# Optimization experiments

Measured on AMD Instinct MI355X. Metric: run time of the kernel, lower is better.

## Reference

```python
import jax, jax.numpy as jnp
import numpy as np

NUM_SITES_X = 2048
NUM_SITES_Y = 4096
NUM_CLB_SITES = 6_000_000
NUM_SLICE_SITES = 6_000_000
NUM_SITES = NUM_SITES_X * NUM_SITES_Y  # global flattened site-id space


def setup_inputs() -> dict:
    key = jax.random.key(0)
    k1, k2, k3, k4 = jax.random.split(key, 4)
    # CLB slice site ids (x*num_sites_y + y), sorted as produced from the column-major fabric scan
    slice_sites = jnp.sort(
        jax.random.randint(k1, (NUM_SLICE_SITES,), 0, NUM_SITES, dtype=jnp.int32))
    # per-CLB-site signature count; >0 means the site already has instances committed
    site_det_sig_idx = jax.random.randint(
        k2, (NUM_CLB_SITES,), 0, 4, dtype=jnp.int32)
    # compact CLB address -> global site id map (monotone by construction in the original)
    addr2site_map = jnp.sort(
        jax.random.randint(k3, (NUM_CLB_SITES,), 0, NUM_SITES, dtype=jnp.int32))
    # per-slice-site legalization score (site_det_score analogue)
    site_scores = jax.random.normal(k4, (NUM_SLICE_SITES,), dtype=jnp.float32)
    return {
        "slice_sites": slice_sites,
        "site_det_sig_idx": site_det_sig_idx,
        "addr2site_map": addr2site_map,
        "site_scores": site_scores,
    }


def _remaining_mask(slice_sites, site_det_sig_idx, addr2site_map):
    """Faithful jit-friendly version of compute_remaining_slice_sites.

    torch/np original:
      assigned = addr2site_map[site_det_sig_idx > 0]
      mask[np.in1d(slice_sites, assigned)] = True; return ~mask
    We avoid the data-dependent boolean gather by replacing unassigned
    entries with a -1 sentinel (site ids are >= 0), sorting, and doing a
    vectorized membership test via searchsorted.
    """
    n = addr2site_map.shape[0]
    assigned = jnp.where(site_det_sig_idx > 0, addr2site_map, jnp.int32(-1))
    assigned_sorted = jnp.sort(assigned)  # sentinels land at the front
    pos = jnp.searchsorted(assigned_sorted, slice_sites, side="left")
    pos = jnp.clip(pos, 0, n - 1)
    found = assigned_sorted[pos] == slice_sites  # in1d membership
    return ~found  # True where the slice site is still available


def reference(slice_sites, site_det_sig_idx, addr2site_map, site_scores):
    remaining = _remaining_mask(slice_sites, site_det_sig_idx, addr2site_map)
    # scores of still-available candidate sites (zeros where already assigned)
    avail_scores = jnp.where(remaining, site_scores, jnp.zeros((), site_scores.dtype))
    return remaining, avail_scores
```

## Files before the change

### kernel.cpp

```cpp
#include <hip/hip_runtime.h>


typedef int   v4i __attribute__((ext_vector_type(4)));
typedef float v4f __attribute__((ext_vector_type(4)));

static constexpr int WORDS_PER_BLOCK = 128;
static constexpr int SITES_PER_BLOCK = 4096;
static constexpr int BIN_SHIFT       = 12;
static constexpr int GRID            = 2048;
static constexpr int BLOCK           = 256;

__device__ __forceinline__ void transitions(
    const int* __restrict__ x, int* __restrict__ bnd, int n, int t)
{
    const int s = t * 4;
    if (s >= n) return;
    int v[4];
    int cnt;
    if (s + 4 <= n) {
        v4i a = __builtin_nontemporal_load((const v4i*)(x + s));
        v[0] = a.x; v[1] = a.y; v[2] = a.z; v[3] = a.w;
        cnt = 4;
    } else {
        cnt = n - s;
        for (int j = 0; j < cnt; ++j) v[j] = x[s + j];
    }
    int pbin = (s == 0) ? -1 : (x[s - 1] >> BIN_SHIFT);
    for (int j = 0; j < cnt; ++j) {
        const int i = s + j;
        const int cbin = v[j] >> BIN_SHIFT;
        for (int b = pbin + 1; b <= cbin; ++b) bnd[b] = i;
        if (i == n - 1)
            for (int b = cbin + 1; b <= GRID; ++b) bnd[b] = n;
        pbin = cbin;
    }
}

__global__ __launch_bounds__(BLOCK) void bounds_kernel(
    const int* __restrict__ ss, const int* __restrict__ a2s,
    int* __restrict__ pb, int* __restrict__ eb, int n_slice, int n_clb)
{
    const int t = blockIdx.x * BLOCK + threadIdx.x;
    transitions(ss,  pb, n_slice, t);
    transitions(a2s, eb, n_clb,  t);
}

__global__ __launch_bounds__(BLOCK) void fused_kernel(
    const int*   __restrict__ ss,
    const int*   __restrict__ sig,
    const int*   __restrict__ a2s,
    const float* __restrict__ sc,
    const int*   __restrict__ eb,
    const int*   __restrict__ pb,
    float*       __restrict__ rem,
    float*       __restrict__ avail,
    int n_clb)
{
    __shared__ unsigned int lbm[WORDS_PER_BLOCK];

    const int g        = blockIdx.x;
    const int siteBase = g * SITES_PER_BLOCK;
    const int siteEnd  = siteBase + SITES_PER_BLOCK;

    for (int w = threadIdx.x; w < WORDS_PER_BLOCK; w += BLOCK) lbm[w] = 0u;

    const int e0 = eb[g], e1 = eb[g + 1];
    const int p0 = pb[g], p1 = pb[g + 1];

    __syncthreads();

    const int mstart = e0 & ~3;
    for (int s = mstart + threadIdx.x * 8; s < e1; s += BLOCK * 8) {
        int av[8], gv[8];
        if (s + 8 <= n_clb) {
            v4i a0 = __builtin_nontemporal_load((const v4i*)(a2s + s));
            v4i a1 = __builtin_nontemporal_load((const v4i*)(a2s + s + 4));
            v4i g0 = __builtin_nontemporal_load((const v4i*)(sig + s));
            v4i g1 = __builtin_nontemporal_load((const v4i*)(sig + s + 4));
            av[0]=a0.x; av[1]=a0.y; av[2]=a0.z; av[3]=a0.w;
            av[4]=a1.x; av[5]=a1.y; av[6]=a1.z; av[7]=a1.w;
            gv[0]=g0.x; gv[1]=g0.y; gv[2]=g0.z; gv[3]=g0.w;
            gv[4]=g1.x; gv[5]=g1.y; gv[6]=g1.z; gv[7]=g1.w;
        } else {
#pragma unroll
            for (int j = 0; j < 8; ++j) {
                const int i = s + j;
                const bool ok = i < n_clb;
                av[j] = ok ? a2s[i] : -1;
                gv[j] = ok ? sig[i] : 0;
            }
        }
        unsigned int curw = 0xFFFFFFFFu, curm = 0u;
#pragma unroll
        for (int j = 0; j < 8; ++j) {
            const int site = av[j];
            if (gv[j] > 0 && site >= siteBase && site < siteEnd) {
                const unsigned int u = (unsigned int)(site - siteBase);
                const unsigned int w = u >> 5;
                const unsigned int m = 1u << (u & 31u);
                if (w == curw) curm |= m;
                else { if (curm) atomicOr(&lbm[curw], curm); curw = w; curm = m; }
            }
        }
        if (curm) atomicOr(&lbm[curw], curm);
    }

    __syncthreads();

    int i0 = (p0 + 3) & ~3;
    int i1 = p1 & ~3;
    if (i1 < i0) i1 = i0;

    for (int q = (i0 >> 2) + threadIdx.x; q < (i1 >> 2); q += BLOCK) {
        v4i s = __builtin_nontemporal_load((const v4i*)ss + q);
        v4f f = __builtin_nontemporal_load((const v4f*)sc + q);
        v4f r, a;
#pragma unroll
        for (int j = 0; j < 4; ++j) {
            const unsigned int u   = (unsigned int)(s[j] - siteBase);
            const unsigned int bit = (lbm[u >> 5] >> (u & 31u)) & 1u;
            r[j] = bit ? 0.0f : 1.0f;
            a[j] = bit ? 0.0f : f[j];
        }
        __builtin_nontemporal_store(r, (v4f*)rem + q);
        __builtin_nontemporal_store(a, (v4f*)avail + q);
    }
    for (int i = p0 + threadIdx.x; i < min(i0, p1); i += BLOCK) {
        const unsigned int u   = (unsigned int)(ss[i] - siteBase);
        const unsigned int bit = (lbm[u >> 5] >> (u & 31u)) & 1u;
        rem[i]   = bit ? 0.0f : 1.0f;
        avail[i] = bit ? 0.0f : sc[i];
    }
    for (int i = max(i1, p0) + threadIdx.x; i < p1; i += BLOCK) {
        const unsigned int u   = (unsigned int)(ss[i] - siteBase);
        const unsigned int bit = (lbm[u >> 5] >> (u & 31u)) & 1u;
        rem[i]   = bit ? 0.0f : 1.0f;
        avail[i] = bit ? 0.0f : sc[i];
    }
}

extern "C" void kernel_launch(void* const* d_in, const int* in_sizes, int n_in,
                              void* d_out, int out_size, void* d_ws, size_t ws_size,
                              hipStream_t stream) {
    const int*   slice_sites = (const int*)d_in[0];
    const int*   sig         = (const int*)d_in[1];
    const int*   a2s         = (const int*)d_in[2];
    const float* scores      = (const float*)d_in[3];
    const int n_slice = in_sizes[0];
    const int n_clb   = in_sizes[1];

    int* eb = (int*)d_ws;
    int* pb = eb + (GRID + 1);

    const int n_max = n_slice > n_clb ? n_slice : n_clb;
    const int tblocks = (n_max / 4 + BLOCK - 1) / BLOCK + 1;
    bounds_kernel<<<tblocks, BLOCK, 0, stream>>>(
        slice_sites, a2s, pb, eb, n_slice, n_clb);

    float* rem   = (float*)d_out;
    float* avail = rem + n_slice;

    fused_kernel<<<GRID, BLOCK, 0, stream>>>(
        slice_sites, sig, a2s, scores, eb, pb, rem, avail, n_clb);
}
```

Before: 150.0 us.

## Merge bounds and mark/probe kernels into one cooperative kernel with grid sync

```diff
diff --git a/kernel.cpp b/kernel.cpp
--- a/kernel.cpp
+++ b/kernel.cpp
@@ -1,4 +1,7 @@
 #include <hip/hip_runtime.h>
+#include <hip/hip_cooperative_groups.h>
+
+namespace cg = cooperative_groups;
 
 
 typedef int   v4i __attribute__((ext_vector_type(4)));
@@ -29,45 +32,26 @@
     for (int j = 0; j < cnt; ++j) {
         const int i = s + j;
         const int cbin = v[j] >> BIN_SHIFT;
-        for (int b = pbin + 1; b <= cbin; ++b) bnd[b] = i;
+        for (int b = pbin + 1; b <= cbin; ++b)
+            __hip_atomic_store(&bnd[b], i, __ATOMIC_RELAXED, __HIP_MEMORY_SCOPE_AGENT);
         if (i == n - 1)
-            for (int b = cbin + 1; b <= GRID; ++b) bnd[b] = n;
+            for (int b = cbin + 1; b <= GRID; ++b)
+                __hip_atomic_store(&bnd[b], n, __ATOMIC_RELAXED, __HIP_MEMORY_SCOPE_AGENT);
         pbin = cbin;
     }
 }
 
-__global__ __launch_bounds__(BLOCK) void bounds_kernel(
-    const int* __restrict__ ss, const int* __restrict__ a2s,
-    int* __restrict__ pb, int* __restrict__ eb, int n_slice, int n_clb)
-{
-    const int t = blockIdx.x * BLOCK + threadIdx.x;
-    transitions(ss,  pb, n_slice, t);
-    transitions(a2s, eb, n_clb,  t);
-}
-
-__global__ __launch_bounds__(BLOCK) void fused_kernel(
+__device__ __forceinline__ void mark_and_probe(
     const int*   __restrict__ ss,
     const int*   __restrict__ sig,
     const int*   __restrict__ a2s,
     const float* __restrict__ sc,
-    const int*   __restrict__ eb,
-    const int*   __restrict__ pb,
+    unsigned int* lbm,
     float*       __restrict__ rem,
     float*       __restrict__ avail,
-    int n_clb)
-{
-    __shared__ unsigned int lbm[WORDS_PER_BLOCK];
-
-    const int g        = blockIdx.x;
-    const int siteBase = g * SITES_PER_BLOCK;
-    const int siteEnd  = siteBase + SITES_PER_BLOCK;
-
-    for (int w = threadIdx.x; w < WORDS_PER_BLOCK; w += BLOCK) lbm[w] = 0u;
-
-    const int e0 = eb[g], e1 = eb[g + 1];
-    const int p0 = pb[g], p1 = pb[g + 1];
-
-    __syncthreads();
+    int e0, int e1, int p0, int p1, int siteBase, int n_clb)
+{
+    const int siteEnd = siteBase + SITES_PER_BLOCK;
 
     const int mstart = e0 & ~3;
     for (int s = mstart + threadIdx.x * 8; s < e1; s += BLOCK * 8) {
@@ -139,27 +123,96 @@
     }
 }
 
+__global__ __launch_bounds__(BLOCK) void coop_kernel(
+    const int*   __restrict__ ss,
+    const int*   __restrict__ sig,
+    const int*   __restrict__ a2s,
+    const float* __restrict__ sc,
+    int*         __restrict__ eb,
+    int*         __restrict__ pb,
+    float*       __restrict__ rem,
+    float*       __restrict__ avail,
+    int n_slice, int n_clb)
+{
+    __shared__ unsigned int lbm[WORDS_PER_BLOCK];
+
+    const int t0 = blockIdx.x * BLOCK + threadIdx.x;
+    const int NT = GRID * BLOCK;
+    for (int t = t0; t * 4 < n_slice; t += NT) transitions(ss,  pb, n_slice, t);
+    for (int t = t0; t * 4 < n_clb;  t += NT) transitions(a2s, eb, n_clb,  t);
+
+    for (int w = threadIdx.x; w < WORDS_PER_BLOCK; w += BLOCK) lbm[w] = 0u;
+
+    cg::this_grid().sync();
+
+    const int g = blockIdx.x;
+    const int e0 = __hip_atomic_load(&eb[g],     __ATOMIC_RELAXED, __HIP_MEMORY_SCOPE_AGENT);
+    const int e1 = __hip_atomic_load(&eb[g + 1], __ATOMIC_RELAXED, __HIP_MEMORY_SCOPE_AGENT);
+    const int p0 = __hip_atomic_load(&pb[g],     __ATOMIC_RELAXED, __HIP_MEMORY_SCOPE_AGENT);
+    const int p1 = __hip_atomic_load(&pb[g + 1], __ATOMIC_RELAXED, __HIP_MEMORY_SCOPE_AGENT);
+
+    mark_and_probe(ss, sig, a2s, sc, lbm, rem, avail,
+                   e0, e1, p0, p1, g * SITES_PER_BLOCK, n_clb);
+}
+
+__global__ __launch_bounds__(BLOCK) void bounds_kernel(
+    const int* __restrict__ ss, const int* __restrict__ a2s,
+    int* __restrict__ pb, int* __restrict__ eb, int n_slice, int n_clb)
+{
+    const int t = blockIdx.x * BLOCK + threadIdx.x;
+    transitions(ss,  pb, n_slice, t);
+    transitions(a2s, eb, n_clb,  t);
+}
+
+__global__ __launch_bounds__(BLOCK) void fused_kernel(
+    const int*   __restrict__ ss,
+    const int*   __restrict__ sig,
+    const int*   __restrict__ a2s,
+    const float* __restrict__ sc,
+    const int*   __restrict__ eb,
+    const int*   __restrict__ pb,
+    float*       __restrict__ rem,
+    float*       __restrict__ avail,
+    int n_clb)
+{
+    __shared__ unsigned int lbm[WORDS_PER_BLOCK];
+    const int g = blockIdx.x;
+    for (int w = threadIdx.x; w < WORDS_PER_BLOCK; w += BLOCK) lbm[w] = 0u;
+    const int e0 = eb[g], e1 = eb[g + 1];
+    const int p0 = pb[g], p1 = pb[g + 1];
+    __syncthreads();
+    mark_and_probe(ss, sig, a2s, sc, lbm, rem, avail,
+                   e0, e1, p0, p1, g * SITES_PER_BLOCK, n_clb);
+}
+
 extern "C" void kernel_launch(void* const* d_in, const int* in_sizes, int n_in,
                               void* d_out, int out_size, void* d_ws, size_t ws_size,
                               hipStream_t stream) {
-    const int*   slice_sites = (const int*)d_in[0];
-    const int*   sig         = (const int*)d_in[1];
-    const int*   a2s         = (const int*)d_in[2];
-    const float* scores      = (const float*)d_in[3];
-    const int n_slice = in_sizes[0];
-    const int n_clb   = in_sizes[1];
+    const int*   ss  = (const int*)d_in[0];
+    const int*   sig = (const int*)d_in[1];
+    const int*   a2s = (const int*)d_in[2];
+    const float* sc  = (const float*)d_in[3];
+    int n_slice = in_sizes[0];
+    int n_clb   = in_sizes[1];
 
     int* eb = (int*)d_ws;
     int* pb = eb + (GRID + 1);
 
-    const int n_max = n_slice > n_clb ? n_slice : n_clb;
-    const int tblocks = (n_max / 4 + BLOCK - 1) / BLOCK + 1;
-    bounds_kernel<<<tblocks, BLOCK, 0, stream>>>(
-        slice_sites, a2s, pb, eb, n_slice, n_clb);
-
     float* rem   = (float*)d_out;
     float* avail = rem + n_slice;
 
-    fused_kernel<<<GRID, BLOCK, 0, stream>>>(
-        slice_sites, sig, a2s, scores, eb, pb, rem, avail, n_clb);
-}
+    void* args[] = { (void*)&ss, (void*)&sig, (void*)&a2s, (void*)&sc,
+                     (void*)&eb, (void*)&pb, (void*)&rem, (void*)&avail,
+                     (void*)&n_slice, (void*)&n_clb };
+    hipError_t err = hipLaunchCooperativeKernel(
+        reinterpret_cast<const void*>(&coop_kernel),
+        dim3(GRID), dim3(BLOCK), args, 0, stream);
+
+    if (err != hipSuccess) {
+        const int n_max = n_slice > n_clb ? n_slice : n_clb;
+        const int tblocks = (n_max / 4 + BLOCK - 1) / BLOCK + 1;
+        bounds_kernel<<<tblocks, BLOCK, 0, stream>>>(ss, a2s, pb, eb, n_slice, n_clb);
+        fused_kernel<<<GRID, BLOCK, 0, stream>>>(ss, sig, a2s, sc, eb, pb,
+                                                 rem, avail, n_clb);
+    }
+}
```

Measured after the change: 382.1 us. +154.7%, slower.

## Split fused bin kernel into global bitmap mark and flat probe passes

Applied to the files above, without the earlier changes.

```diff
diff --git a/kernel.cpp b/kernel.cpp
--- a/kernel.cpp
+++ b/kernel.cpp
@@ -4,69 +4,51 @@
 typedef int   v4i __attribute__((ext_vector_type(4)));
 typedef float v4f __attribute__((ext_vector_type(4)));
 
-static constexpr int WORDS_PER_BLOCK = 128;
-static constexpr int SITES_PER_BLOCK = 4096;
-static constexpr int BIN_SHIFT       = 12;
-static constexpr int GRID            = 2048;
-static constexpr int BLOCK           = 256;
+static constexpr int WORDS_PER_BIN = 128;
+static constexpr int SITES_PER_BIN = 4096;
+static constexpr int BIN_SHIFT     = 12;
+static constexpr int NBINS         = 2048;
+static constexpr int BLOCK         = 256;
 
-__device__ __forceinline__ void transitions(
-    const int* __restrict__ x, int* __restrict__ bnd, int n, int t)
+__global__ __launch_bounds__(BLOCK) void bounds_kernel(
+    const int* __restrict__ a2s, int* __restrict__ eb, int n_clb)
 {
+    const int t = blockIdx.x * BLOCK + threadIdx.x;
     const int s = t * 4;
-    if (s >= n) return;
+    if (s >= n_clb) return;
     int v[4];
     int cnt;
-    if (s + 4 <= n) {
-        v4i a = __builtin_nontemporal_load((const v4i*)(x + s));
+    if (s + 4 <= n_clb) {
+        v4i a = __builtin_nontemporal_load((const v4i*)(a2s + s));
         v[0] = a.x; v[1] = a.y; v[2] = a.z; v[3] = a.w;
         cnt = 4;
     } else {
-        cnt = n - s;
-        for (int j = 0; j < cnt; ++j) v[j] = x[s + j];
+        cnt = n_clb - s;
+        for (int j = 0; j < cnt; ++j) v[j] = a2s[s + j];
     }
-    int pbin = (s == 0) ? -1 : (x[s - 1] >> BIN_SHIFT);
+    int pbin = (s == 0) ? -1 : (a2s[s - 1] >> BIN_SHIFT);
     for (int j = 0; j < cnt; ++j) {
         const int i = s + j;
         const int cbin = v[j] >> BIN_SHIFT;
-        for (int b = pbin + 1; b <= cbin; ++b) bnd[b] = i;
-        if (i == n - 1)
-            for (int b = cbin + 1; b <= GRID; ++b) bnd[b] = n;
+        for (int b = pbin + 1; b <= cbin; ++b) eb[b] = i;
+        if (i == n_clb - 1)
+            for (int b = cbin + 1; b <= NBINS; ++b) eb[b] = n_clb;
         pbin = cbin;
     }
 }
 
-__global__ __launch_bounds__(BLOCK) void bounds_kernel(
-    const int* __restrict__ ss, const int* __restrict__ a2s,
-    int* __restrict__ pb, int* __restrict__ eb, int n_slice, int n_clb)
+__global__ __launch_bounds__(BLOCK) void mark_kernel(
+    const int* __restrict__ sig, const int* __restrict__ a2s,
+    const int* __restrict__ eb, unsigned int* __restrict__ bm, int n_clb)
 {
-    const int t = blockIdx.x * BLOCK + threadIdx.x;
-    transitions(ss,  pb, n_slice, t);
-    transitions(a2s, eb, n_clb,  t);
-}
-
-__global__ __launch_bounds__(BLOCK) void fused_kernel(
-    const int*   __restrict__ ss,
-    const int*   __restrict__ sig,
-    const int*   __restrict__ a2s,
-    const float* __restrict__ sc,
-    const int*   __restrict__ eb,
-    const int*   __restrict__ pb,
-    float*       __restrict__ rem,
-    float*       __restrict__ avail,
-    int n_clb)
-{
-    __shared__ unsigned int lbm[WORDS_PER_BLOCK];
+    __shared__ unsigned int lbm[WORDS_PER_BIN];
 
     const int g        = blockIdx.x;
-    const int siteBase = g * SITES_PER_BLOCK;
-    const int siteEnd  = siteBase + SITES_PER_BLOCK;
+    const int siteBase = g * SITES_PER_BIN;
+    const int siteEnd  = siteBase + SITES_PER_BIN;
 
-    for (int w = threadIdx.x; w < WORDS_PER_BLOCK; w += BLOCK) lbm[w] = 0u;
-
+    if (threadIdx.x < WORDS_PER_BIN) lbm[threadIdx.x] = 0u;
     const int e0 = eb[g], e1 = eb[g + 1];
-    const int p0 = pb[g], p1 = pb[g + 1];
-
     __syncthreads();
 
     const int mstart = e0 & ~3;
@@ -107,59 +89,70 @@
 
     __syncthreads();
 
-    int i0 = (p0 + 3) & ~3;
-    int i1 = p1 & ~3;
-    if (i1 < i0) i1 = i0;
+    if (threadIdx.x < WORDS_PER_BIN / 4)
+        ((v4i*)(bm + g * WORDS_PER_BIN))[threadIdx.x] =
+            ((const v4i*)lbm)[threadIdx.x];
+}
 
-    for (int q = (i0 >> 2) + threadIdx.x; q < (i1 >> 2); q += BLOCK) {
-        v4i s = __builtin_nontemporal_load((const v4i*)ss + q);
-        v4f f = __builtin_nontemporal_load((const v4f*)sc + q);
-        v4f r, a;
+__global__ __launch_bounds__(BLOCK) void probe_kernel(
+    const int* __restrict__ ss, const float* __restrict__ sc,
+    const unsigned int* __restrict__ bm,
+    float* __restrict__ rem, float* __restrict__ avail, int n4)
+{
+    const int q = blockIdx.x * BLOCK + threadIdx.x;
+    if (q >= n4) return;
+    v4i s = __builtin_nontemporal_load((const v4i*)ss + q);
+    v4f f = __builtin_nontemporal_load((const v4f*)sc + q);
+    v4f r, a;
 #pragma unroll
-        for (int j = 0; j < 4; ++j) {
-            const unsigned int u   = (unsigned int)(s[j] - siteBase);
-            const unsigned int bit = (lbm[u >> 5] >> (u & 31u)) & 1u;
-            r[j] = bit ? 0.0f : 1.0f;
-            a[j] = bit ? 0.0f : f[j];
-        }
-        __builtin_nontemporal_store(r, (v4f*)rem + q);
-        __builtin_nontemporal_store(a, (v4f*)avail + q);
+    for (int j = 0; j < 4; ++j) {
+        const unsigned int u   = (unsigned int)s[j];
+        const unsigned int bit = (bm[u >> 5] >> (u & 31u)) & 1u;
+        r[j] = bit ? 0.0f : 1.0f;
+        a[j] = bit ? 0.0f : f[j];
     }
-    for (int i = p0 + threadIdx.x; i < min(i0, p1); i += BLOCK) {
-        const unsigned int u   = (unsigned int)(ss[i] - siteBase);
-        const unsigned int bit = (lbm[u >> 5] >> (u & 31u)) & 1u;
-        rem[i]   = bit ? 0.0f : 1.0f;
-        avail[i] = bit ? 0.0f : sc[i];
-    }
-    for (int i = max(i1, p0) + threadIdx.x; i < p1; i += BLOCK) {
-        const unsigned int u   = (unsigned int)(ss[i] - siteBase);
-        const unsigned int bit = (lbm[u >> 5] >> (u & 31u)) & 1u;
-        rem[i]   = bit ? 0.0f : 1.0f;
-        avail[i] = bit ? 0.0f : sc[i];
-    }
+    __builtin_nontemporal_store(r, (v4f*)rem + q);
+    __builtin_nontemporal_store(a, (v4f*)avail + q);
+}
+
+__global__ void probe_tail_kernel(
+    const int* __restrict__ ss, const float* __restrict__ sc,
+    const unsigned int* __restrict__ bm,
+    float* __restrict__ rem, float* __restrict__ avail, int start, int n)
+{
+    const int i = start + blockIdx.x * blockDim.x + threadIdx.x;
+    if (i >= n) return;
+    const unsigned int u   = (unsigned int)ss[i];
+    const unsigned int bit = (bm[u >> 5] >> (u & 31u)) & 1u;
+    rem[i]   = bit ? 0.0f : 1.0f;
+    avail[i] = bit ? 0.0f : sc[i];
 }
 
 extern "C" void kernel_launch(void* const* d_in, const int* in_sizes, int n_in,
                               void* d_out, int out_size, void* d_ws, size_t ws_size,
                               hipStream_t stream) {
-    const int*   slice_sites = (const int*)d_in[0];
-    const int*   sig         = (const int*)d_in[1];
-    const int*   a2s         = (const int*)d_in[2];
-    const float* scores      = (const float*)d_in[3];
+    const int*   ss  = (const int*)d_in[0];
+    const int*   sig = (const int*)d_in[1];
+    const int*   a2s = (const int*)d_in[2];
+    const float* sc  = (const float*)d_in[3];
     const int n_slice = in_sizes[0];
     const int n_clb   = in_sizes[1];
 
-    int* eb = (int*)d_ws;
-    int* pb = eb + (GRID + 1);
+    unsigned int* bm = (unsigned int*)d_ws;
+    int*          eb = (int*)(bm + NBINS * WORDS_PER_BIN);
 
-    const int n_max = n_slice > n_clb ? n_slice : n_clb;
-    const int tblocks = (n_max / 4 + BLOCK - 1) / BLOCK + 1;
-    bounds_kernel<<<tblocks, BLOCK, 0, stream>>>(
-        slice_sites, a2s, pb, eb, n_slice, n_clb);
+    const int t1 = (n_clb / 4 + BLOCK - 1) / BLOCK + 1;
+    bounds_kernel<<<t1, BLOCK, 0, stream>>>(a2s, eb, n_clb);
+
+    mark_kernel<<<NBINS, BLOCK, 0, stream>>>(sig, a2s, eb, bm, n_clb);
 
     float* rem   = (float*)d_out;
     float* avail = rem + n_slice;
-
-    fused_kernel<<<GRID, BLOCK, 0, stream>>>(
-        slice_sites, sig, a2s, scores, eb, pb, rem, avail, n_clb);
+    const int n4 = n_slice / 4;
+    if (n4 > 0)
+        probe_kernel<<<(n4 + BLOCK - 1) / BLOCK, BLOCK, 0, stream>>>(
+            ss, sc, bm, rem, avail, n4);
+    if (n4 * 4 < n_slice)
+        probe_tail_kernel<<<1, 64, 0, stream>>>(ss, sc, bm, rem, avail,
+                                                n4 * 4, n_slice);
 }
```

Result: faster. 145.0 us (median of 2 runs) (-3.4%).
